# Performance work log

Hardware: AMD Instinct MI355X
Metric: run time of the kernel (lower is better)

The kernel has to match this reference:

```python
import jax, jax.numpy as jnp
import numpy as np
from math import log

N = 100000          # num_nodes
D = 128             # emb_dimension
NEG = 5             # negatives per node
LR = 0.025
NCE_BIAS = log(N)
NCE_NEG_BIAS = log(N / NEG)
LUT_SIZE = 1202     # len(arange(-6.01, 6.01, 0.01))


def make_lookup_table():
    t = jax.nn.sigmoid(jnp.arange(-6.01, 6.01, 0.01, dtype=jnp.float32))
    t = t.at[0].set(0.0).at[-1].set(1.0)
    return t


def fast_sigmoid(score, lookup_table):
    idx = jnp.floor((score + 6.01) / 0.01).astype(jnp.int32)
    idx = jnp.clip(idx, 0, LUT_SIZE - 1)  # guard float rounding at +/-6
    return jnp.take(lookup_table, idx)


def setup_inputs() -> dict:
    key = jax.random.key(0)
    k1, k2, k3, k4, k5 = jax.random.split(key, 5)
    W = jax.random.uniform(k1, (N, D), dtype=jnp.float32, minval=-0.5, maxval=0.5)
    lookup_table = make_lookup_table()
    idx_pos_u = jax.random.randint(k2, (N,), 0, N)
    idx_pos_v = jax.random.randint(k3, (N,), 0, N)
    idx_neg_u = jnp.repeat(idx_pos_u, NEG)  # matches sample_index: same u repeated per negative
    idx_neg_v = jax.random.randint(k5, (N * NEG,), 0, N)
    return {"W": W, "lookup_table": lookup_table,
            "idx_pos_u": idx_pos_u, "idx_pos_v": idx_pos_v,
            "idx_neg_u": idx_neg_u, "idx_neg_v": idx_neg_v}


def reference(W, lookup_table, idx_pos_u, idx_pos_v, idx_neg_u, idx_neg_v):
    # ---- positive pairs: gather, dot, LUT-sigmoid, scatter-add ----
    emb_pos_u = W[idx_pos_u]                       # [N, D]
    emb_pos_v = W[idx_pos_v]                       # [N, D]
    pos_score = jnp.sum(emb_pos_u * emb_pos_v, axis=1) - NCE_BIAS
    pos_score = jnp.clip(pos_score, -6.0, 6.0)
    score = ((1.0 - fast_sigmoid(pos_score, lookup_table)) * LR)[:, None]
    W = W.at[idx_pos_u].add(score * emb_pos_v)
    W = W.at[idx_pos_v].add(score * emb_pos_u)
    # ---- negative pairs: gathers read the UPDATED table (as in torch code) ----
    emb_neg_u = W[idx_neg_u]                       # [N*NEG, D]
    emb_neg_v = W[idx_neg_v]                       # [N*NEG, D]
    neg_score = jnp.sum(emb_neg_u * emb_neg_v, axis=1) - NCE_NEG_BIAS
    neg_score = jnp.clip(neg_score, -6.0, 6.0)
    score = (0.0 - fast_sigmoid(neg_score, lookup_table) * LR)[:, None]
    W = W.at[idx_neg_u].add(score * emb_neg_v)
    W = W.at[idx_neg_v].add(score * emb_neg_u)
    return W
```

## Files before the change

kernel.cpp:

```cpp
#include <hip/hip_runtime.h>
#include <hip/hip_bf16.h>

#define D 128
#define LR 0.025f
#define NCE_BIAS 11.512925464970229f
#define NCE_NEG_BIAS 9.903487552536127f
#define LUT_SIZE 1202

__device__ __forceinline__ float wave_allreduce(float x) {
    #pragma unroll
    for (int m = 32; m >= 1; m >>= 1) x += __shfl_xor(x, m, 64);
    return x;
}

__device__ __forceinline__ float fast_sig(float x) {
    x = fminf(fmaxf(x, -6.0f), 6.0f) - 0.005f;
    float e = __expf(-x);
    return __builtin_amdgcn_rcpf(1.0f + e);
}

__device__ __forceinline__ float fast_sig_lut(float s, const float* __restrict__ lut) {
    s = fminf(fmaxf(s, -6.0f), 6.0f);
    int idx = (int)floorf((s + 6.01f) / 0.01f);
    idx = min(max(idx, 0), LUT_SIZE - 1);
    return lut[idx];
}

__device__ __forceinline__ unsigned int bf16_rne(float f) {
    unsigned int u = __float_as_uint(f);
    return (u + 0x7FFFu + ((u >> 16) & 1u)) >> 16;
}

__global__ __launch_bounds__(256) void hist_kernel(
    const int* __restrict__ ipu, const int* __restrict__ ipv,
    const int* __restrict__ inu, const int* __restrict__ inv,
    int Np, int Nn, int NEG, int* __restrict__ cnt)
{
    int t = blockIdx.x * 256 + threadIdx.x;
    if (t < Np) {
        int u = inu[(size_t)NEG * t];
        atomicAdd(&cnt[u], 1 + (NEG << 16));
        atomicAdd(&cnt[ipu[t]], 0);
    } else if (t < Np + Nn) {
        int k = t - Np;
        atomicAdd(&cnt[inv[k]], 1 << 16);
    }
}

__global__ __launch_bounds__(256) void hist_kernel2(
    const int* __restrict__ ipv, int Np, int* __restrict__ cnt)
{
    int t = blockIdx.x * 256 + threadIdx.x;
    if (t < Np) atomicAdd(&cnt[ipv[t]], 1);
}

__global__ __launch_bounds__(256) void scan_local(
    const int* __restrict__ cnt, int* __restrict__ off, int* __restrict__ bsum,
    int n, int shift)
{
    __shared__ int sh[256];
    int g = blockIdx.x * 256 + threadIdx.x;
    int x = (g < n) ? ((cnt[g] >> shift) & 0xFFFF) : 0;
    sh[threadIdx.x] = x;
    __syncthreads();
    #pragma unroll
    for (int d = 1; d < 256; d <<= 1) {
        int t = (threadIdx.x >= d) ? sh[threadIdx.x - d] : 0;
        __syncthreads();
        sh[threadIdx.x] += t;
        __syncthreads();
    }
    if (g < n) off[g] = sh[threadIdx.x] - x;
    if (threadIdx.x == 255) bsum[blockIdx.x] = sh[255];
}

__global__ __launch_bounds__(256) void scan_bsum(int* __restrict__ bsum, int nb)
{
    __shared__ int sh[256];
    __shared__ int carry_s;
    if (threadIdx.x == 0) carry_s = 0;
    __syncthreads();
    for (int c = 0; c < nb; c += 256) {
        int i = c + threadIdx.x;
        int x = (i < nb) ? bsum[i] : 0;
        sh[threadIdx.x] = x;
        __syncthreads();
        for (int d = 1; d < 256; d <<= 1) {
            int t = (threadIdx.x >= d) ? sh[threadIdx.x - d] : 0;
            __syncthreads();
            sh[threadIdx.x] += t;
            __syncthreads();
        }
        int carry = carry_s;
        if (i < nb) bsum[i] = sh[threadIdx.x] - x + carry;
        __syncthreads();
        if (threadIdx.x == 0) carry_s = carry + sh[255];
        __syncthreads();
    }
}

__global__ __launch_bounds__(256) void add_base(
    int* __restrict__ off, int* __restrict__ cur, const int* __restrict__ bsum, int n)
{
    int g = blockIdx.x * 256 + threadIdx.x;
    if (g < n) {
        int v = off[g] + bsum[blockIdx.x];
        off[g] = v;
        cur[g] = v;
    }
}

__global__ __launch_bounds__(256) void fill_kernel(
    const int* __restrict__ ipu, const int* __restrict__ ipv,
    const int* __restrict__ inu, const int* __restrict__ inv,
    int Np, int Nn, int NEG,
    int* __restrict__ cur_p, int* __restrict__ cur_n,
    int* __restrict__ ent_p, int* __restrict__ ent_n)
{
    int t = blockIdx.x * 256 + threadIdx.x;
    if (t < Np) {
        int u = ipu[t], v = ipv[t];
        ent_p[atomicAdd(&cur_p[u], 1)] = v;
        ent_p[atomicAdd(&cur_p[v], 1)] = u;
        int un = inu[(size_t)NEG * t];
        int ns = atomicAdd(&cur_n[un], NEG);
        for (int j = 0; j < NEG; ++j)
            ent_n[ns + j] = inv[(size_t)NEG * t + j];
    } else if (t < Np + Nn) {
        int k = t - Np;
        ent_n[atomicAdd(&cur_n[inv[k]], 1)] = inu[k];
    }
}

template<bool BF16P, bool EMIT16>
__global__ __launch_bounds__(256) void update_kernel(
    const float* __restrict__ baseSrc,
    const float* __restrict__ partnerF,
    const unsigned short* __restrict__ partnerH,
    float* __restrict__ dst,
    unsigned short* __restrict__ dst16,
    const int* __restrict__ off, const int* __restrict__ cur,
    const int* __restrict__ entries,
    int N, float bias, float cpos)
{
    int gtid = blockIdx.x * 256 + threadIdx.x;
    int node = gtid >> 5;
    int hl   = threadIdx.x & 31;
    if (node >= N) return;

    float4 base = ((const float4*)baseSrc)[(size_t)node * 32 + hl];
    float ax = 0.0f, ay = 0.0f, az = 0.0f, aw = 0.0f;

    int beg = off[node];
    int len = cur[node] - beg;

    for (int g = 0; g < len; g += 4) {
        float4 r[4];
        float d[4];
        #pragma unroll
        for (int i = 0; i < 4; ++i) {
            int t = g + i;
            int p = (t < len) ? entries[beg + t] : node;
            if (BF16P) {
                uint2 raw = ((const uint2*)partnerH)[(size_t)p * 32 + hl];
                r[i].x = __uint_as_float(raw.x << 16);
                r[i].y = __uint_as_float(raw.x & 0xFFFF0000u);
                r[i].z = __uint_as_float(raw.y << 16);
                r[i].w = __uint_as_float(raw.y & 0xFFFF0000u);
            } else {
                r[i] = ((const float4*)partnerF)[(size_t)p * 32 + hl];
            }
        }
        #pragma unroll
        for (int i = 0; i < 4; ++i)
            d[i] = r[i].x * base.x + r[i].y * base.y + r[i].z * base.z + r[i].w * base.w;
        #pragma unroll
        for (int m = 16; m >= 1; m >>= 1) {
            #pragma unroll
            for (int i = 0; i < 4; ++i) d[i] += __shfl_xor(d[i], m, 64);
        }
        #pragma unroll
        for (int i = 0; i < 4; ++i) {
            float s = (g + i < len) ? (cpos - fast_sig(d[i] - bias)) * LR : 0.0f;
            ax += s * r[i].x;
            ay += s * r[i].y;
            az += s * r[i].z;
            aw += s * r[i].w;
        }
    }
    float4 o = make_float4(base.x + ax, base.y + ay, base.z + az, base.w + aw);
    ((float4*)dst)[(size_t)node * 32 + hl] = o;
    if (EMIT16) {
        uint2 h;
        h.x = bf16_rne(o.x) | (bf16_rne(o.y) << 16);
        h.y = bf16_rne(o.z) | (bf16_rne(o.w) << 16);
        ((uint2*)dst16)[(size_t)node * 32 + hl] = h;
    }
}

__global__ __launch_bounds__(256) void pos_kernel(
    const float* __restrict__ Worig, float* __restrict__ W,
    const float* __restrict__ lut,
    const int* __restrict__ idx_u, const int* __restrict__ idx_v, int n)
{
    int wave = (int)((blockIdx.x * blockDim.x + threadIdx.x) >> 6);
    int lane = threadIdx.x & 63;
    if (wave >= n) return;
    int u = idx_u[wave];
    int v = idx_v[wave];
    float2 eu = ((const float2*)(Worig + (size_t)u * D))[lane];
    float2 ev = ((const float2*)(Worig + (size_t)v * D))[lane];
    float dot = wave_allreduce(eu.x * ev.x + eu.y * ev.y);
    float s = (1.0f - fast_sig_lut(dot - NCE_BIAS, lut)) * LR;
    float* wu = W + (size_t)u * D;
    float* wv = W + (size_t)v * D;
    atomicAdd(&wu[2 * lane],     s * ev.x);
    atomicAdd(&wu[2 * lane + 1], s * ev.y);
    atomicAdd(&wv[2 * lane],     s * eu.x);
    atomicAdd(&wv[2 * lane + 1], s * eu.y);
}

__global__ __launch_bounds__(256) void neg_kernel(
    const float* __restrict__ Wsnap, float* __restrict__ W,
    const float* __restrict__ lut,
    const int* __restrict__ idx_u, const int* __restrict__ idx_v, int n, int neg)
{
    int wave = (int)((blockIdx.x * blockDim.x + threadIdx.x) >> 6);
    int lane = threadIdx.x & 63;
    if (wave >= n) return;
    int u = idx_u[wave * neg];
    float2 eu = ((const float2*)(Wsnap + (size_t)u * D))[lane];
    float dux = 0.0f, duy = 0.0f;
    for (int j = 0; j < neg; ++j) {
        int v = idx_v[wave * neg + j];
        float2 ev = ((const float2*)(Wsnap + (size_t)v * D))[lane];
        float dot = wave_allreduce(eu.x * ev.x + eu.y * ev.y);
        float s = -fast_sig_lut(dot - NCE_NEG_BIAS, lut) * LR;
        dux += s * ev.x;
        duy += s * ev.y;
        float* wv = W + (size_t)v * D;
        atomicAdd(&wv[2 * lane],     s * eu.x);
        atomicAdd(&wv[2 * lane + 1], s * eu.y);
    }
    float* wu = W + (size_t)u * D;
    atomicAdd(&wu[2 * lane],     dux);
    atomicAdd(&wu[2 * lane + 1], duy);
}

extern "C" void kernel_launch(void* const* d_in, const int* in_sizes, int n_in,
                              void* d_out, int out_size, void* d_ws, size_t ws_size,
                              hipStream_t stream) {
    const float* W   = (const float*)d_in[0];
    const float* lut = (const float*)d_in[1];
    const int* ipu   = (const int*)d_in[2];
    const int* ipv   = (const int*)d_in[3];
    const int* inu   = (const int*)d_in[4];
    const int* inv   = (const int*)d_in[5];
    float* out = (float*)d_out;

    const int N  = in_sizes[0] / D;
    const int Np = in_sizes[2];
    const int Nn = in_sizes[4];
    const int NEG = Nn / Np;
    const size_t WB = (size_t)N * D * sizeof(float);
    const int nb = (N + 255) / 256;
    const int n_entp = 2 * Np;
    const int n_entn = NEG * Np + Nn;

    size_t need = (size_t)N * D * 2
                + (size_t)n_entp * 4 + (size_t)n_entn * 4
                + (size_t)N * 4 * 5
                + (size_t)nb * 4 * 2 + 64;

    if (ws_size >= need) {
        char* p = (char*)d_ws;
        unsigned short* ws16 = (unsigned short*)p; p += (size_t)N * D * 2;
        int* ent_p = (int*)p; p += (size_t)n_entp * 4;
        int* ent_n = (int*)p; p += (size_t)n_entn * 4;
        int* cnt   = (int*)p; p += (size_t)N * 4;
        int* off_p = (int*)p; p += (size_t)N * 4;
        int* off_n = (int*)p; p += (size_t)N * 4;
        int* cur_p = (int*)p; p += (size_t)N * 4;
        int* cur_n = (int*)p; p += (size_t)N * 4;
        int* bsA   = (int*)p; p += (size_t)nb * 4;
        int* bsB   = (int*)p;

        hipMemsetAsync(cnt, 0, (size_t)N * 4, stream);
        int tot = Np + Nn;
        hist_kernel <<<(tot + 255) / 256, 256, 0, stream>>>(ipu, ipv, inu, inv, Np, Nn, NEG, cnt);
        hist_kernel2<<<(Np + 255) / 256, 256, 0, stream>>>(ipv, Np, cnt);
        scan_local<<<nb, 256, 0, stream>>>(cnt, off_p, bsA, N, 0);
        scan_bsum<<<1, 256, 0, stream>>>(bsA, nb);
        add_base<<<nb, 256, 0, stream>>>(off_p, cur_p, bsA, N);
        scan_local<<<nb, 256, 0, stream>>>(cnt, off_n, bsB, N, 16);
        scan_bsum<<<1, 256, 0, stream>>>(bsB, nb);
        add_base<<<nb, 256, 0, stream>>>(off_n, cur_n, bsB, N);
        fill_kernel<<<(tot + 255) / 256, 256, 0, stream>>>(ipu, ipv, inu, inv, Np, Nn, NEG,
                                                           cur_p, cur_n, ent_p, ent_n);

        int ublocks = (N * 32 + 255) / 256;
        update_kernel<false, true><<<ublocks, 256, 0, stream>>>(
            W, W, (const unsigned short*)nullptr, out, ws16,
            off_p, cur_p, ent_p, N, NCE_BIAS, 1.0f);
        update_kernel<true, false><<<ublocks, 256, 0, stream>>>(
            out, (const float*)nullptr, ws16, out, (unsigned short*)nullptr,
            off_n, cur_n, ent_n, N, NCE_NEG_BIAS, 0.0f);
    } else {
        float* snap = (float*)d_ws;
        hipMemcpyAsync(out, W, WB, hipMemcpyDeviceToDevice, stream);
        int blocks = (Np * 64 + 255) / 256;
        pos_kernel<<<blocks, 256, 0, stream>>>(W, out, lut, ipu, ipv, Np);
        hipMemcpyAsync(snap, out, WB, hipMemcpyDeviceToDevice, stream);
        neg_kernel<<<blocks, 256, 0, stream>>>(snap, out, lut, inu, inv, Np, NEG);
    }
}
```

Measured before the change: 312.5 us.

## Merge CSR build passes, prefetch bf16 partner rows, use bf16 for positive phase

The two count/scan/add-base chains are merged into single kernels that work on int2 (positive, negative) counters, using 64-bit atomics to bump both counters at once. A conversion kernel writes a bf16 copy of W so the positive-phase update also gathers bf16 partner rows instead of fp32, halving its gather bytes. The update loop now software-pipelines, preloading the next group's partner rows and the indices two groups ahead so gather latency overlaps with compute. In exchange it adds a full-table conversion pass and extra workspace, and the positive phase now loses precision because partner values are rounded to bf16.

```diff
diff --git a/kernel.cpp b/kernel.cpp
--- a/kernel.cpp
+++ b/kernel.cpp
@@ -31,58 +31,71 @@
     return (u + 0x7FFFu + ((u >> 16) & 1u)) >> 16;
 }
 
+__global__ __launch_bounds__(256) void conv_kernel(
+    const float* __restrict__ W, unsigned short* __restrict__ w16, int n32)
+{
+    int g = blockIdx.x * 256 + threadIdx.x;
+    if (g >= n32) return;
+    float4 v = ((const float4*)W)[g];
+    uint2 h;
+    h.x = bf16_rne(v.x) | (bf16_rne(v.y) << 16);
+    h.y = bf16_rne(v.z) | (bf16_rne(v.w) << 16);
+    ((uint2*)w16)[g] = h;
+}
+
 __global__ __launch_bounds__(256) void hist_kernel(
     const int* __restrict__ ipu, const int* __restrict__ ipv,
-    const int* __restrict__ inu, const int* __restrict__ inv,
-    int Np, int Nn, int NEG, int* __restrict__ cnt)
+    const int* __restrict__ inv,
+    int Np, int Nn, int NEG, int2* __restrict__ cnt2)
 {
     int t = blockIdx.x * 256 + threadIdx.x;
     if (t < Np) {
-        int u = inu[(size_t)NEG * t];
-        atomicAdd(&cnt[u], 1 + (NEG << 16));
-        atomicAdd(&cnt[ipu[t]], 0);
+        atomicAdd((unsigned long long*)&cnt2[ipu[t]],
+                  1ull + ((unsigned long long)NEG << 32));
+        atomicAdd(&cnt2[ipv[t]].x, 1);
     } else if (t < Np + Nn) {
         int k = t - Np;
-        atomicAdd(&cnt[inv[k]], 1 << 16);
-    }
-}
-
-__global__ __launch_bounds__(256) void hist_kernel2(
-    const int* __restrict__ ipv, int Np, int* __restrict__ cnt)
-{
-    int t = blockIdx.x * 256 + threadIdx.x;
-    if (t < Np) atomicAdd(&cnt[ipv[t]], 1);
-}
-
-__global__ __launch_bounds__(256) void scan_local(
-    const int* __restrict__ cnt, int* __restrict__ off, int* __restrict__ bsum,
-    int n, int shift)
-{
-    __shared__ int sh[256];
+        atomicAdd(&cnt2[inv[k]].y, 1);
+    }
+}
+
+__global__ __launch_bounds__(256) void scan_local2(
+    const int2* __restrict__ cnt2, int* __restrict__ off_p, int* __restrict__ off_n,
+    int* __restrict__ bsp, int* __restrict__ bsn, int n)
+{
+    __shared__ int shp[256], shn[256];
     int g = blockIdx.x * 256 + threadIdx.x;
-    int x = (g < n) ? ((cnt[g] >> shift) & 0xFFFF) : 0;
-    sh[threadIdx.x] = x;
+    int2 x = (g < n) ? cnt2[g] : make_int2(0, 0);
+    shp[threadIdx.x] = x.x;
+    shn[threadIdx.x] = x.y;
     __syncthreads();
     #pragma unroll
     for (int d = 1; d < 256; d <<= 1) {
-        int t = (threadIdx.x >= d) ? sh[threadIdx.x - d] : 0;
-        __syncthreads();
-        sh[threadIdx.x] += t;
-        __syncthreads();
-    }
-    if (g < n) off[g] = sh[threadIdx.x] - x;
-    if (threadIdx.x == 255) bsum[blockIdx.x] = sh[255];
-}
-
-__global__ __launch_bounds__(256) void scan_bsum(int* __restrict__ bsum, int nb)
-{
+        int tp = (threadIdx.x >= d) ? shp[threadIdx.x - d] : 0;
+        int tn = (threadIdx.x >= d) ? shn[threadIdx.x - d] : 0;
+        __syncthreads();
+        shp[threadIdx.x] += tp;
+        shn[threadIdx.x] += tn;
+        __syncthreads();
+    }
+    if (g < n) {
+        off_p[g] = shp[threadIdx.x] - x.x;
+        off_n[g] = shn[threadIdx.x] - x.y;
+    }
+    if (threadIdx.x == 255) {
+        bsp[blockIdx.x] = shp[255];
+        bsn[blockIdx.x] = shn[255];
+    }
+}
+
+__device__ __forceinline__ void scan_one(int* b, int nb) {
     __shared__ int sh[256];
     __shared__ int carry_s;
     if (threadIdx.x == 0) carry_s = 0;
     __syncthreads();
     for (int c = 0; c < nb; c += 256) {
         int i = c + threadIdx.x;
-        int x = (i < nb) ? bsum[i] : 0;
+        int x = (i < nb) ? b[i] : 0;
         sh[threadIdx.x] = x;
         __syncthreads();
         for (int d = 1; d < 256; d <<= 1) {
@@ -92,21 +105,31 @@
             __syncthreads();
         }
         int carry = carry_s;
-        if (i < nb) bsum[i] = sh[threadIdx.x] - x + carry;
+        if (i < nb) b[i] = sh[threadIdx.x] - x + carry;
         __syncthreads();
         if (threadIdx.x == 0) carry_s = carry + sh[255];
         __syncthreads();
     }
 }
 
-__global__ __launch_bounds__(256) void add_base(
-    int* __restrict__ off, int* __restrict__ cur, const int* __restrict__ bsum, int n)
+__global__ __launch_bounds__(256) void scan_bsum2(int* __restrict__ bsp, int* __restrict__ bsn, int nb)
+{
+    scan_one(bsp, nb);
+    __syncthreads();
+    scan_one(bsn, nb);
+}
+
+__global__ __launch_bounds__(256) void add_base2(
+    int* __restrict__ off_p, int* __restrict__ off_n, int2* __restrict__ cur2,
+    const int* __restrict__ bsp, const int* __restrict__ bsn, int n)
 {
     int g = blockIdx.x * 256 + threadIdx.x;
     if (g < n) {
-        int v = off[g] + bsum[blockIdx.x];
-        off[g] = v;
-        cur[g] = v;
+        int vp = off_p[g] + bsp[blockIdx.x];
+        int vn = off_n[g] + bsn[blockIdx.x];
+        off_p[g] = vp;
+        off_n[g] = vn;
+        cur2[g] = make_int2(vp, vn);
     }
 }
 
@@ -114,34 +137,32 @@
     const int* __restrict__ ipu, const int* __restrict__ ipv,
     const int* __restrict__ inu, const int* __restrict__ inv,
     int Np, int Nn, int NEG,
-    int* __restrict__ cur_p, int* __restrict__ cur_n,
-    int* __restrict__ ent_p, int* __restrict__ ent_n)
+    int2* __restrict__ cur2, int* __restrict__ ent_p, int* __restrict__ ent_n)
 {
     int t = blockIdx.x * 256 + threadIdx.x;
     if (t < Np) {
         int u = ipu[t], v = ipv[t];
-        ent_p[atomicAdd(&cur_p[u], 1)] = v;
-        ent_p[atomicAdd(&cur_p[v], 1)] = u;
-        int un = inu[(size_t)NEG * t];
-        int ns = atomicAdd(&cur_n[un], NEG);
+        unsigned long long pk = atomicAdd((unsigned long long*)&cur2[u],
+                                          1ull + ((unsigned long long)NEG << 32));
+        int slot_pu = (int)(pk & 0xFFFFFFFFull);
+        int slot_nu = (int)(pk >> 32);
+        ent_p[slot_pu] = v;
         for (int j = 0; j < NEG; ++j)
-            ent_n[ns + j] = inv[(size_t)NEG * t + j];
+            ent_n[slot_nu + j] = inv[(size_t)NEG * t + j];
+        ent_p[atomicAdd(&cur2[v].x, 1)] = u;
     } else if (t < Np + Nn) {
         int k = t - Np;
-        ent_n[atomicAdd(&cur_n[inv[k]], 1)] = inu[k];
-    }
-}
-
-template<bool BF16P, bool EMIT16>
+        ent_n[atomicAdd(&cur2[inv[k]].y, 1)] = inu[k];
+    }
+}
+
+template<bool EMIT16>
 __global__ __launch_bounds__(256) void update_kernel(
     const float* __restrict__ baseSrc,
-    const float* __restrict__ partnerF,
     const unsigned short* __restrict__ partnerH,
-    float* __restrict__ dst,
-    unsigned short* __restrict__ dst16,
-    const int* __restrict__ off, const int* __restrict__ cur,
-    const int* __restrict__ entries,
-    int N, float bias, float cpos)
+    float* __restrict__ dst, unsigned short* __restrict__ dst16,
+    const int* __restrict__ offArr, const int* __restrict__ endArr2, int comp,
+    const int* __restrict__ entries, int N, float bias, float cpos)
 {
     int gtid = blockIdx.x * 256 + threadIdx.x;
     int node = gtid >> 5;
@@ -151,41 +172,60 @@
     float4 base = ((const float4*)baseSrc)[(size_t)node * 32 + hl];
     float ax = 0.0f, ay = 0.0f, az = 0.0f, aw = 0.0f;
 
-    int beg = off[node];
-    int len = cur[node] - beg;
-
-    for (int g = 0; g < len; g += 4) {
-        float4 r[4];
-        float d[4];
+    int beg = offArr[node];
+    int len = endArr2[2 * node + comp] - beg;
+    const uint2* ph = (const uint2*)partnerH;
+
+    if (len > 0) {
+        int gcount = (len + 3) >> 2;
+        int en[4];
+        uint2 rc[4];
         #pragma unroll
         for (int i = 0; i < 4; ++i) {
-            int t = g + i;
-            int p = (t < len) ? entries[beg + t] : node;
-            if (BF16P) {
-                uint2 raw = ((const uint2*)partnerH)[(size_t)p * 32 + hl];
-                r[i].x = __uint_as_float(raw.x << 16);
-                r[i].y = __uint_as_float(raw.x & 0xFFFF0000u);
-                r[i].z = __uint_as_float(raw.y << 16);
-                r[i].w = __uint_as_float(raw.y & 0xFFFF0000u);
-            } else {
-                r[i] = ((const float4*)partnerF)[(size_t)p * 32 + hl];
-            }
-        }
-        #pragma unroll
-        for (int i = 0; i < 4; ++i)
-            d[i] = r[i].x * base.x + r[i].y * base.y + r[i].z * base.z + r[i].w * base.w;
-        #pragma unroll
-        for (int m = 16; m >= 1; m >>= 1) {
-            #pragma unroll
-            for (int i = 0; i < 4; ++i) d[i] += __shfl_xor(d[i], m, 64);
+            int t = min(i, len - 1);
+            rc[i] = ph[(size_t)entries[beg + t] * 32 + hl];
         }
         #pragma unroll
         for (int i = 0; i < 4; ++i) {
-            float s = (g + i < len) ? (cpos - fast_sig(d[i] - bias)) * LR : 0.0f;
-            ax += s * r[i].x;
-            ay += s * r[i].y;
-            az += s * r[i].z;
-            aw += s * r[i].w;
+            int t = min(4 + i, len - 1);
+            en[i] = entries[beg + t];
+        }
+        for (int g = 0; g < gcount; ++g) {
+            uint2 rn[4];
+            #pragma unroll
+            for (int i = 0; i < 4; ++i) rn[i] = ph[(size_t)en[i] * 32 + hl];
+            int en2[4];
+            #pragma unroll
+            for (int i = 0; i < 4; ++i) {
+                int t = (g + 2) * 4 + i;
+                t = (t < len) ? t : (len - 1);
+                en2[i] = entries[beg + t];
+            }
+            float4 r[4];
+            float d[4];
+            #pragma unroll
+            for (int i = 0; i < 4; ++i) {
+                r[i].x = __uint_as_float(rc[i].x << 16);
+                r[i].y = __uint_as_float(rc[i].x & 0xFFFF0000u);
+                r[i].z = __uint_as_float(rc[i].y << 16);
+                r[i].w = __uint_as_float(rc[i].y & 0xFFFF0000u);
+                d[i] = r[i].x * base.x + r[i].y * base.y + r[i].z * base.z + r[i].w * base.w;
+            }
+            #pragma unroll
+            for (int m = 16; m >= 1; m >>= 1) {
+                #pragma unroll
+                for (int i = 0; i < 4; ++i) d[i] += __shfl_xor(d[i], m, 64);
+            }
+            #pragma unroll
+            for (int i = 0; i < 4; ++i) {
+                float s = (g * 4 + i < len) ? (cpos - fast_sig(d[i] - bias)) * LR : 0.0f;
+                ax += s * r[i].x;
+                ay += s * r[i].y;
+                az += s * r[i].z;
+                aw += s * r[i].w;
+            }
+            #pragma unroll
+            for (int i = 0; i < 4; ++i) { rc[i] = rn[i]; en[i] = en2[i]; }
         }
     }
     float4 o = make_float4(base.x + ax, base.y + ay, base.z + az, base.w + aw);
@@ -267,44 +307,41 @@
     const int n_entp = 2 * Np;
     const int n_entn = NEG * Np + Nn;
 
-    size_t need = (size_t)N * D * 2
+    size_t need = (size_t)N * D * 2 * 2
                 + (size_t)n_entp * 4 + (size_t)n_entn * 4
-                + (size_t)N * 4 * 5
+                + (size_t)N * 8 * 2 + (size_t)N * 4 * 2
                 + (size_t)nb * 4 * 2 + 64;
 
     if (ws_size >= need) {
         char* p = (char*)d_ws;
-        unsigned short* ws16 = (unsigned short*)p; p += (size_t)N * D * 2;
-        int* ent_p = (int*)p; p += (size_t)n_entp * 4;
-        int* ent_n = (int*)p; p += (size_t)n_entn * 4;
-        int* cnt   = (int*)p; p += (size_t)N * 4;
-        int* off_p = (int*)p; p += (size_t)N * 4;
-        int* off_n = (int*)p; p += (size_t)N * 4;
-        int* cur_p = (int*)p; p += (size_t)N * 4;
-        int* cur_n = (int*)p; p += (size_t)N * 4;
-        int* bsA   = (int*)p; p += (size_t)nb * 4;
-        int* bsB   = (int*)p;
-
-        hipMemsetAsync(cnt, 0, (size_t)N * 4, stream);
+        unsigned short* w16W = (unsigned short*)p; p += (size_t)N * D * 2;
+        unsigned short* w16P = (unsigned short*)p; p += (size_t)N * D * 2;
+        int*  ent_p = (int*)p;  p += (size_t)n_entp * 4;
+        int*  ent_n = (int*)p;  p += (size_t)n_entn * 4;
+        int2* cnt2  = (int2*)p; p += (size_t)N * 8;
+        int2* cur2  = (int2*)p; p += (size_t)N * 8;
+        int*  off_p = (int*)p;  p += (size_t)N * 4;
+        int*  off_n = (int*)p;  p += (size_t)N * 4;
+        int*  bsp   = (int*)p;  p += (size_t)nb * 4;
+        int*  bsn   = (int*)p;
+
+        hipMemsetAsync(cnt2, 0, (size_t)N * 8, stream);
+        int n32 = N * 32;
+        conv_kernel<<<(n32 + 255) / 256, 256, 0, stream>>>(W, w16W, n32);
         int tot = Np + Nn;
-        hist_kernel <<<(tot + 255) / 256, 256, 0, stream>>>(ipu, ipv, inu, inv, Np, Nn, NEG, cnt);
-        hist_kernel2<<<(Np + 255) / 256, 256, 0, stream>>>(ipv, Np, cnt);
-        scan_local<<<nb, 256, 0, stream>>>(cnt, off_p, bsA, N, 0);
-        scan_bsum<<<1, 256, 0, stream>>>(bsA, nb);
-        add_base<<<nb, 256, 0, stream>>>(off_p, cur_p, bsA, N);
-        scan_local<<<nb, 256, 0, stream>>>(cnt, off_n, bsB, N, 16);
-        scan_bsum<<<1, 256, 0, stream>>>(bsB, nb);
-        add_base<<<nb, 256, 0, stream>>>(off_n, cur_n, bsB, N);
+        hist_kernel<<<(tot + 255) / 256, 256, 0, stream>>>(ipu, ipv, inv, Np, Nn, NEG, cnt2);
+        scan_local2<<<nb, 256, 0, stream>>>(cnt2, off_p, off_n, bsp, bsn, N);
+        scan_bsum2<<<1, 256, 0, stream>>>(bsp, bsn, nb);
+        add_base2<<<nb, 256, 0, stream>>>(off_p, off_n, cur2, bsp, bsn, N);
         fill_kernel<<<(tot + 255) / 256, 256, 0, stream>>>(ipu, ipv, inu, inv, Np, Nn, NEG,
-                                                           cur_p, cur_n, ent_p, ent_n);
-
-        int ublocks = (N * 32 + 255) / 256;
-        update_kernel<false, true><<<ublocks, 256, 0, stream>>>(
-            W, W, (const unsigned short*)nullptr, out, ws16,
-            off_p, cur_p, ent_p, N, NCE_BIAS, 1.0f);
-        update_kernel<true, false><<<ublocks, 256, 0, stream>>>(
-            out, (const float*)nullptr, ws16, out, (unsigned short*)nullptr,
-            off_n, cur_n, ent_n, N, NCE_NEG_BIAS, 0.0f);
+                                                           cur2, ent_p, ent_n);
+
+        int ublocks = (n32 + 255) / 256;
+        update_kernel<true><<<ublocks, 256, 0, stream>>>(
+            W, w16W, out, w16P, off_p, (const int*)cur2, 0, ent_p, N, NCE_BIAS, 1.0f);
+        update_kernel<false><<<ublocks, 256, 0, stream>>>(
+            out, w16P, out, (unsigned short*)nullptr, off_n, (const int*)cur2, 1, ent_n,
+            N, NCE_NEG_BIAS, 0.0f);
     } else {
         float* snap = (float*)d_ws;
         hipMemcpyAsync(out, W, WB, hipMemcpyDeviceToDevice, stream);
```

After: 272.4 us. 12.8% less time.
